# Kernel tuning notes

Measured on AMD Instinct MI355X. Metric: run time of the kernel, lower is better.

The kernel has to match this reference:

```python
import jax, jax.numpy as jnp
import numpy as np
from jax import lax

NUM_CLASSES = 91
C_FEAT = 2048
HF = WF = 16          # backbone feature map size (512px image / stride 32)
STRIDE = 32           # anchor stride, as in source generate_base_anchors
N_ANCHOR_TYPES = 9
NMS_THR = 0.5
K_ROIS = 100          # fixed proposal count after NMS (padded, jit-safe)
SPATIAL_SCALE = 1.0 / 16.0
POOL = 7
SR = 2                # sampling ratio (source uses adaptive -1; fixed here)


def conv2d(x, w, b, pad):
    y = lax.conv_general_dilated(x, w, (1, 1), pad,
                                 dimension_numbers=('NCHW', 'OIHW', 'NCHW'))
    return y + b[None, :, None, None]


def setup_inputs():
    key = jax.random.key(0)
    ks = jax.random.split(key, 16)
    f32 = jnp.float32
    def w(k, shape, s=0.01):
        return jax.random.normal(k, shape, f32) * s
    z = lambda n: jnp.zeros((n,), f32)
    D = C_FEAT * POOL * POOL  # 100352
    return dict(
        x=jax.random.normal(ks[0], (1, C_FEAT, HF, WF), f32),
        rpn_w=w(ks[1], (512, C_FEAT, 3, 3)), rpn_b=z(512),
        cls_w=w(ks[2], (18, 512, 1, 1)), cls_b=z(18),
        bbox_w=w(ks[3], (36, 512, 1, 1)), bbox_b=z(36),
        fc1c_w=w(ks[4], (D, 4096)), fc1c_b=z(4096),
        fc2c_w=w(ks[5], (4096, NUM_CLASSES)), fc2c_b=z(NUM_CLASSES),
        fc1b_w=w(ks[6], (D, 4096)), fc1b_b=z(4096),
        fc2b_w=w(ks[7], (4096, 4)), fc2b_b=z(4),
        m1_w=w(ks[8], (256, C_FEAT, 3, 3)), m1_b=z(256),
        mt_w=w(ks[9], (256, 256, 2, 2)), mt_b=z(256),  # ConvT weight [C_in,C_out,kh,kw]
        m2_w=w(ks[10], (1, 256, 1, 1)), m2_b=z(1),
    )


def _anchors(hf, wf):
    scales = jnp.array([8.0, 16.0, 32.0])
    ratios = jnp.array([0.5, 1.0, 2.0])
    ws = (scales[:, None] * jnp.sqrt(ratios)[None, :]).reshape(-1)  # scale-major, 9
    hs = (scales[:, None] / jnp.sqrt(ratios)[None, :]).reshape(-1)
    base = jnp.stack([-ws / 2, -hs / 2, ws / 2, hs / 2], axis=1)    # [9,4]
    sy, sx = jnp.meshgrid(jnp.arange(hf) * STRIDE, jnp.arange(wf) * STRIDE, indexing='ij')
    shifts = jnp.stack([sx, sy, sx, sy], -1).reshape(-1, 4).astype(jnp.float32)  # [HW,4]
    return (base[:, None, :] + shifts[None, :, :]).reshape(-1, 4)   # [9*HW,4] anchor-type major


def _decode(a, d):
    wa = a[:, 2] - a[:, 0]
    ha = a[:, 3] - a[:, 1]
    cx = a[:, 0] + 0.5 * wa
    cy = a[:, 1] + 0.5 * ha
    px = cx + d[:, 0] * wa
    py = cy + d[:, 1] * ha
    pw = jnp.exp(d[:, 2]) * wa
    ph = jnp.exp(d[:, 3]) * ha
    return jnp.stack([px - 0.5 * pw, py - 0.5 * ph, px + 0.5 * pw, py + 0.5 * ph], 1)


def _nms_topk(boxes, scores, thr, k):
    n = boxes.shape[0]
    order = jnp.argsort(-scores)
    b = boxes[order]
    s = scores[order]
    area = (b[:, 2] - b[:, 0]) * (b[:, 3] - b[:, 1])
    xx1 = jnp.maximum(b[:, None, 0], b[None, :, 0])
    yy1 = jnp.maximum(b[:, None, 1], b[None, :, 1])
    xx2 = jnp.minimum(b[:, None, 2], b[None, :, 2])
    yy2 = jnp.minimum(b[:, None, 3], b[None, :, 3])
    inter = jnp.clip(xx2 - xx1, 0) * jnp.clip(yy2 - yy1, 0)
    iou = inter / (area[:, None] + area[None, :] - inter + 1e-9)
    j = jnp.arange(n)
    def body(i, keep):
        sup = keep[i] & (iou[i] > thr) & (j > i)
        return keep & ~sup
    keep = lax.fori_loop(0, n, body, jnp.ones((n,), bool))
    masked = jnp.where(keep, s, -jnp.inf)
    vals, pos = lax.top_k(masked, k)
    valid = jnp.isfinite(vals)
    fb = jnp.where(valid[:, None], b[pos], 0.0)
    fs = jnp.where(valid, vals, 0.0)
    return fb, fs


def _roi_align(feat, boxes):
    # feat: [C,H,W]; boxes: [K,4] in image coords
    C, H, W = feat.shape
    r = boxes * SPATIAL_SCALE
    S = POOL * SR  # 14 sample points per side
    t = (jnp.arange(S, dtype=feat.dtype) + 0.5) / S
    gx = jnp.clip(r[:, 0:1] + t[None, :] * (r[:, 2:3] - r[:, 0:1]), 0.0, W - 1.0)
    gy = jnp.clip(r[:, 1:2] + t[None, :] * (r[:, 3:4] - r[:, 1:2]), 0.0, H - 1.0)
    x0 = jnp.floor(gx); y0 = jnp.floor(gy)
    lx = gx - x0; ly = gy - y0
    x0i = x0.astype(jnp.int32); y0i = y0.astype(jnp.int32)
    x1i = jnp.minimum(x0i + 1, W - 1); y1i = jnp.minimum(y0i + 1, H - 1)
    flat = feat.reshape(C, H * W)
    def g(yi, xi):  # yi:[K,S] row coords, xi:[K,S] col coords -> [C,K,S,S]
        idx = yi[:, :, None] * W + xi[:, None, :]
        return flat[:, idx]
    lyb = ly[:, :, None]; lxb = lx[:, None, :]
    v = ((1 - lyb) * (1 - lxb) * g(y0i, x0i)
         + (1 - lyb) * lxb * g(y0i, x1i)
         + lyb * (1 - lxb) * g(y1i, x0i)
         + lyb * lxb * g(y1i, x1i))  # [C,K,S,S]
    v = v.reshape(C, -1, POOL, SR, POOL, SR).mean(axis=(3, 5))
    return v.transpose(1, 0, 2, 3)  # [K,C,7,7]


def reference(x, rpn_w, rpn_b, cls_w, cls_b, bbox_w, bbox_b,
              fc1c_w, fc1c_b, fc2c_w, fc2c_b,
              fc1b_w, fc1b_b, fc2b_w, fc2b_b,
              m1_w, m1_b, mt_w, mt_b, m2_w, m2_b):
    p1 = [(1, 1), (1, 1)]; p0 = [(0, 0), (0, 0)]
    f = jax.nn.relu(conv2d(x, rpn_w, rpn_b, p1))      # [1,512,H,W]
    obj = conv2d(f, cls_w, cls_b, p0)                 # [1,18,H,W]
    deltas = conv2d(f, bbox_w, bbox_b, p0)            # [1,36,H,W]
    hf, wf = f.shape[2], f.shape[3]
    hw = hf * wf
    # softmax over the 2 objectness classes (view(B,2,-1) layout)
    scores = jax.nn.softmax(obj.reshape(2, N_ANCHOR_TYPES, hw), axis=0)[1].reshape(-1)
    d = deltas.reshape(N_ANCHOR_TYPES, 4, hw).transpose(0, 2, 1).reshape(-1, 4)
    anchors = _anchors(hf, wf)
    boxes = _decode(anchors, d)
    fb, fs = _nms_topk(boxes, scores, NMS_THR, K_ROIS)
    rois = _roi_align(x[0], fb)                       # [K,2048,7,7]
    flat = rois.reshape(K_ROIS, -1)
    cls_out = jax.nn.relu(flat @ fc1c_w + fc1c_b) @ fc2c_w + fc2c_b
    box_out = jax.nn.relu(flat @ fc1b_w + fc1b_b) @ fc2b_w + fc2b_b
    m = jax.nn.relu(conv2d(rois, m1_w, m1_b, p1))     # [K,256,7,7]
    # ConvTranspose2d(k=2,s=2): non-overlapping, each pixel expands to a 2x2 block
    up = jnp.einsum('nchw,coij->nohiwj', m, mt_w).reshape(K_ROIS, 256, 2 * POOL, 2 * POOL)
    m = jax.nn.relu(up + mt_b[None, :, None, None])
    masks = conv2d(m, m2_w, m2_b, p0)                 # [K,1,14,14]
    return cls_out, box_out, masks
```

## Files before the change

### kernel.cpp

```cpp
#include <hip/hip_runtime.h>

#define DEVFN __device__ __forceinline__

typedef unsigned short ushort_t;
typedef unsigned int uint32;
typedef __attribute__((ext_vector_type(8))) short bf16x8;
typedef __attribute__((ext_vector_type(4))) float f32x4;

typedef __attribute__((address_space(3))) unsigned int lds_uint;
typedef const __attribute__((address_space(1))) unsigned int glob_uint;

DEVFN ushort_t f2bf(float x) {
    uint32 b = __float_as_uint(x);
    uint32 r = (b + 0x7FFFu + ((b >> 16) & 1u)) >> 16;
    return (ushort_t)r;
}
DEVFN float bf2f(ushort_t u) { return __uint_as_float(((uint32)u) << 16); }

union BWU { uint32 u[4]; bf16x8 v8; };

__global__ __launch_bounds__(256) void k_pre(const float* __restrict__ x,
                                             const float* __restrict__ rpn_w,
                                             float* __restrict__ fpart,
                                             const float* __restrict__ m1_w,
                                             const float* __restrict__ mt_w,
                                             ushort_t* __restrict__ wAf,
                                             ushort_t* __restrict__ wA2f,
                                             float* __restrict__ xt) {
    const int bid = blockIdx.x, tid = threadIdx.x;
    if (bid < 1024) {
        __shared__ float xs[8][18][18];
        const int coP = bid & 127, ks = bid >> 7;
        const int ty = tid >> 4, tx = tid & 15;
        const int co0 = coP * 4;
        for (int i = tid; i < 8 * 18 * 18; i += 256) ((float*)xs)[i] = 0.f;
        float acc[4] = {0.f, 0.f, 0.f, 0.f};
        for (int ch = 0; ch < 32; ++ch) {
            const int cib = ks * 256 + ch * 8;
            __syncthreads();
#pragma unroll
            for (int cc = 0; cc < 8; ++cc) xs[cc][ty + 1][tx + 1] = x[(size_t)(cib + cc) * 256 + tid];
            __syncthreads();
#pragma unroll
            for (int cc = 0; cc < 8; ++cc) {
                const int ci = cib + cc;
                float v[9];
#pragma unroll
                for (int t = 0; t < 9; ++t) v[t] = xs[cc][ty + t / 3][tx + t % 3];
                const float* wb = rpn_w + ((size_t)co0 * 2048 + ci) * 9;
#pragma unroll
                for (int o = 0; o < 4; ++o) {
                    const float* w = wb + (size_t)o * 2048 * 9;
#pragma unroll
                    for (int t = 0; t < 9; ++t) acc[o] = fmaf(v[t], w[t], acc[o]);
                }
            }
        }
#pragma unroll
        for (int o = 0; o < 4; ++o) fpart[((size_t)ks * 512 + co0 + o) * 256 + tid] = acc[o];
        return;
    }
    const int pb = bid - 1024;
    if (pb < 256) {
        const int p = pb * 4 + (tid >> 6);
        const int lane = tid & 63, l15 = lane & 15, lg = lane >> 4;
        const int cot = p >> 6, cis = p & 63;
        const int co = cot * 16 + l15, k0 = cis * 32 + lg * 8;
        const float* src = m1_w + ((size_t)co * 2048 + k0) * 9;
        float v[72];
#pragma unroll
        for (int i = 0; i < 72; ++i) v[i] = src[i];
#pragma unroll
        for (int tap = 0; tap < 9; ++tap) {
            ushort_t* dst = wAf + ((size_t)((tap * 16 + cot) * 64 + cis) * 512) + lane * 8;
            ushort_t t8[8];
#pragma unroll
            for (int j = 0; j < 8; ++j) t8[j] = f2bf(v[j * 9 + tap]);
            uint4 u;
            u.x = (uint32)t8[0] | ((uint32)t8[1] << 16);
            u.y = (uint32)t8[2] | ((uint32)t8[3] << 16);
            u.z = (uint32)t8[4] | ((uint32)t8[5] << 16);
            u.w = (uint32)t8[6] | ((uint32)t8[7] << 16);
            *(uint4*)dst = u;
        }
    } else if (pb < 1280) {
        int idx = (pb - 256) * 256 + tid;
        int j = idx & 7, lane = (idx >> 3) & 63, cis = (idx >> 9) & 7, cot = idx >> 12;
        int row = cot * 16 + (lane & 15);
        int c = cis * 32 + (lane >> 4) * 8 + j;
        int o = row >> 2, ij = row & 3;
        wA2f[idx] = f2bf(mt_w[((size_t)c * 256 + o) * 4 + ij]);
    } else {
        int pos = pb - 1280;
        for (int i = 0; i < 8; ++i) {
            int c = tid + i * 256;
            xt[(size_t)pos * 2048 + c] = x[(size_t)c * 256 + pos];
        }
    }
}

__global__ void k_rpn_reduce(const float* __restrict__ fpart, const float* __restrict__ rpn_b,
                             float* __restrict__ f) {
    const int i = blockIdx.x * 256 + threadIdx.x;
    float s = 0.f;
#pragma unroll
    for (int p = 0; p < 8; ++p) s += fpart[(size_t)p * 131072 + i];
    f[i] = fmaxf(s + rpn_b[i >> 8], 0.f);
}

__global__ void k_head(const float* __restrict__ f, const float* __restrict__ cls_w,
                       const float* __restrict__ cls_b, const float* __restrict__ bbox_w,
                       const float* __restrict__ bbox_b, float* __restrict__ scores,
                       float* __restrict__ boxes) {
    const int a = blockIdx.x, pos = threadIdx.x;
    float o0 = 0, o1 = 0, d0 = 0, d1 = 0, d2 = 0, d3 = 0;
    const float* c0 = cls_w + (size_t)a * 512;
    const float* c1 = cls_w + (size_t)(9 + a) * 512;
    const float* b0p = bbox_w + (size_t)(4 * a) * 512;
    const float* b1p = b0p + 512;
    const float* b2p = b0p + 1024;
    const float* b3p = b0p + 1536;
    for (int ci = 0; ci < 512; ci += 8) {
        float fv[8];
#pragma unroll
        for (int j = 0; j < 8; ++j) fv[j] = f[(size_t)(ci + j) * 256 + pos];
#pragma unroll
        for (int j = 0; j < 8; ++j) {
            o0 = fmaf(c0[ci + j], fv[j], o0);
            o1 = fmaf(c1[ci + j], fv[j], o1);
            d0 = fmaf(b0p[ci + j], fv[j], d0);
            d1 = fmaf(b1p[ci + j], fv[j], d1);
            d2 = fmaf(b2p[ci + j], fv[j], d2);
            d3 = fmaf(b3p[ci + j], fv[j], d3);
        }
    }
    o0 += cls_b[a]; o1 += cls_b[9 + a];
    d0 += bbox_b[4 * a + 0]; d1 += bbox_b[4 * a + 1];
    d2 += bbox_b[4 * a + 2]; d3 += bbox_b[4 * a + 3];
    float mx = fmaxf(o0, o1);
    float e0 = expf(o0 - mx), e1 = expf(o1 - mx);
    float sc = e1 / (e0 + e1);
    int si = a / 3, ri = a % 3;
    float scale = (si == 0) ? 8.f : ((si == 1) ? 16.f : 32.f);
    float ratio = (ri == 0) ? 0.5f : ((ri == 1) ? 1.f : 2.f);
    float sq = sqrtf(ratio);
    float hw2 = (scale * sq) * 0.5f;
    float hh2 = (scale / sq) * 0.5f;
    int py = pos >> 4, px = pos & 15;
    float sx = (float)(px * 32), sy = (float)(py * 32);
    float a0 = sx - hw2, a1 = sy - hh2, a2 = sx + hw2, a3 = sy + hh2;
    float wa = a2 - a0, ha = a3 - a1;
    float cx = a0 + 0.5f * wa, cy = a1 + 0.5f * ha;
    float pxc = cx + d0 * wa, pyc = cy + d1 * ha;
    float pw = expf(d2) * wa, ph = expf(d3) * ha;
    int idx = a * 256 + pos;
    scores[idx] = sc;
    boxes[idx * 4 + 0] = pxc - 0.5f * pw;
    boxes[idx * 4 + 1] = pyc - 0.5f * ph;
    boxes[idx * 4 + 2] = pxc + 0.5f * pw;
    boxes[idx * 4 + 3] = pyc + 0.5f * ph;
}

__global__ void k_sort(const float* __restrict__ scores, const float* __restrict__ boxes,
                       float* __restrict__ ssort, float* __restrict__ bsort) {
    const int i = blockIdx.x * 256 + threadIdx.x;
    const float si = scores[i];
    int rank = 0;
    for (int j = 0; j < 2304; ++j) {
        float sj = scores[j];
        rank += (sj > si) || (sj == si && j < i);
    }
    ssort[rank] = si;
    float4 bb = *(const float4*)(boxes + (size_t)i * 4);
    *(float4*)(bsort + (size_t)rank * 4) = bb;
}

__global__ void k_adj(const float* __restrict__ bsort, unsigned long long* __restrict__ adj) {
    const int i = blockIdx.x, lane = threadIdx.x;
    const float4 bi = *(const float4*)(bsort + (size_t)i * 4);
    const float ai = (bi.z - bi.x) * (bi.w - bi.y);
    for (int w = 0; w < 36; ++w) {
        int j = w * 64 + lane;
        bool sup = false;
        if (j < 2304 && j > i) {
            float4 bj = *(const float4*)(bsort + (size_t)j * 4);
            float aj = (bj.z - bj.x) * (bj.w - bj.y);
            float xx1 = fmaxf(bi.x, bj.x), yy1 = fmaxf(bi.y, bj.y);
            float xx2 = fminf(bi.z, bj.z), yy2 = fminf(bi.w, bj.w);
            float inter = fmaxf(xx2 - xx1, 0.f) * fmaxf(yy2 - yy1, 0.f);
            float iou = inter / (ai + aj - inter + 1e-9f);
            sup = iou > 0.5f;
        }
        unsigned long long m = __ballot(sup);
        if (lane == 0) adj[(size_t)i * 36 + w] = m;
    }
}

__global__ void k_nms(const unsigned long long* __restrict__ adj, const float* __restrict__ bsort,
                      float* __restrict__ fb) {
    const int lane = threadIdx.x;
    unsigned long long r = (lane < 36) ? 0ULL : ~0ULL;
    int cnt = 0;
    for (int it = 0; it < 128; ++it) {
        unsigned long long inv = ~r;
        int local = inv ? (__ffsll((unsigned long long)inv) - 1) : 64;
        int cand = (local < 64) ? lane * 64 + local : (1 << 30);
#pragma unroll
        for (int d = 32; d; d >>= 1) cand = min(cand, __shfl_xor(cand, d));
        if (cand >= 2304) break;
        if (lane == 0) *(float4*)(fb + (size_t)cnt * 4) = *(const float4*)(bsort + (size_t)cand * 4);
        ++cnt;
        if (cnt == 100) break;
        unsigned long long a = (lane < 36) ? adj[(size_t)cand * 36 + lane] : 0ULL;
        r |= a;
        if (lane == (cand >> 6)) r |= 1ULL << (cand & 63);
    }
    for (int s2 = lane; s2 < 100; s2 += 64)
        if (s2 >= cnt) {
            float4 z = {0.f, 0.f, 0.f, 0.f};
            *(float4*)(fb + (size_t)s2 * 4) = z;
        }
}

__global__ __launch_bounds__(256) void k_roi(const float* __restrict__ xt,
                                             const float* __restrict__ fb,
                                             ushort_t* __restrict__ flatA,
                                             ushort_t* __restrict__ flatT) {
    __shared__ int sxi0[14], sxi1[14], syi0[14], syi1[14];
    __shared__ float slx[14], sly[14];
    const int cg = blockIdx.x, n = blockIdx.y, tid = threadIdx.x;
    const float r0 = fb[n * 4 + 0] * 0.0625f, r1 = fb[n * 4 + 1] * 0.0625f;
    const float r2 = fb[n * 4 + 2] * 0.0625f, r3 = fb[n * 4 + 3] * 0.0625f;
    if (tid < 14) {
        float tt = ((float)tid + 0.5f) * (1.0f / 14.0f);
        float gx = r0 + tt * (r2 - r0);
        gx = fminf(fmaxf(gx, 0.f), 15.f);
        float x0f = floorf(gx);
        int x0 = (int)x0f;
        sxi0[tid] = x0; sxi1[tid] = min(x0 + 1, 15); slx[tid] = gx - x0f;
        float gy = r1 + tt * (r3 - r1);
        gy = fminf(fmaxf(gy, 0.f), 15.f);
        float y0f = floorf(gy);
        int y0 = (int)y0f;
        syi0[tid] = y0; syi1[tid] = min(y0 + 1, 15); sly[tid] = gy - y0f;
    }
    __syncthreads();
    const int c = cg * 256 + tid;
    for (int py = 0; py < 7; ++py) {
        for (int px = 0; px < 7; ++px) {
            float accv = 0.f;
#pragma unroll
            for (int a2 = 0; a2 < 2; ++a2) {
                int sy = py * 2 + a2;
                int y0 = syi0[sy], y1 = syi1[sy];
                float ly = sly[sy];
#pragma unroll
                for (int b2 = 0; b2 < 2; ++b2) {
                    int sx = px * 2 + b2;
                    int x0 = sxi0[sx], x1 = sxi1[sx];
                    float lx = slx[sx];
                    float v00 = xt[(size_t)(y0 * 16 + x0) * 2048 + c];
                    float v01 = xt[(size_t)(y0 * 16 + x1) * 2048 + c];
                    float v10 = xt[(size_t)(y1 * 16 + x0) * 2048 + c];
                    float v11 = xt[(size_t)(y1 * 16 + x1) * 2048 + c];
                    accv += (1.f - ly) * (1.f - lx) * v00 + (1.f - ly) * lx * v01 +
                            ly * (1.f - lx) * v10 + ly * lx * v11;
                }
            }
            ushort_t bv = f2bf(accv * 0.25f);
            int pos = py * 7 + px;
            flatT[((size_t)n * 49 + pos) * 2048 + c] = bv;
            int k = c * 49 + pos;
            flatA[((size_t)(k >> 5) * 112 + n) * 32 + (k & 31)] = bv;
        }
    }
}

__global__ __launch_bounds__(256) void k_big(const ushort_t* __restrict__ flatA,
                                             const ushort_t* __restrict__ flatT,
                                             const float* __restrict__ Wc,
                                             const float* __restrict__ Wb,
                                             float* __restrict__ part,
                                             const ushort_t* __restrict__ wAf,
                                             const float* __restrict__ m1_b,
                                             ushort_t* __restrict__ m1outT) {
    __shared__ float wlds[2][32][128];
    const int bid = blockIdx.x, tid = threadIdx.x;
    const int wave = tid >> 6, lane = tid & 63, l15 = lane & 15, lg = lane >> 4;
    const f32x4 zz = {0.f, 0.f, 0.f, 0.f};
    if (bid < 77) {
        const int nb = bid;
        int nn[4], ppy[4], ppx[4], colv[4];
#pragma unroll
        for (int nt = 0; nt < 4; ++nt) {
            int col = nb * 64 + nt * 16 + l15;
            colv[nt] = col;
            int n = col / 49;
            int pos = col - n * 49;
            nn[nt] = n;
            ppy[nt] = pos / 7;
            ppx[nt] = pos - (pos / 7) * 7;
        }
        f32x4 acc[4][4];
#pragma unroll
        for (int a = 0; a < 4; ++a)
#pragma unroll
            for (int b = 0; b < 4; ++b) acc[a][b] = zz;
        bf16x8 zfrag;
#pragma unroll
        for (int j = 0; j < 8; ++j) zfrag[j] = 0;
        for (int tap = 0; tap < 9; ++tap) {
            const int ty = tap / 3 - 1, tx = tap % 3 - 1;
            int val[4];
            size_t bofs[4];
#pragma unroll
            for (int nt = 0; nt < 4; ++nt) {
                int iy = ppy[nt] + ty, ix = ppx[nt] + tx;
                val[nt] = (iy >= 0 && iy < 7 && ix >= 0 && ix < 7);
                bofs[nt] = ((size_t)nn[nt] * 49 + iy * 7 + ix) * 2048;
            }
            for (int cis = 0; cis < 64; ++cis) {
                const int kq = cis * 32 + lg * 8;
                bf16x8 a[4];
#pragma unroll
                for (int mt = 0; mt < 4; ++mt)
                    a[mt] = *(const bf16x8*)(wAf +
                            ((size_t)((tap * 16 + wave * 4 + mt) * 64 + cis) * 64 + lane) * 8);
                bf16x8 b[4];
#pragma unroll
                for (int nt = 0; nt < 4; ++nt)
                    b[nt] = val[nt] ? *(const bf16x8*)(flatT + bofs[nt] + kq) : zfrag;
#pragma unroll
                for (int nt = 0; nt < 4; ++nt)
#pragma unroll
                    for (int mt = 0; mt < 4; ++mt)
                        acc[mt][nt] = __builtin_amdgcn_mfma_f32_16x16x32_bf16(a[mt], b[nt], acc[mt][nt], 0, 0, 0);
            }
        }
#pragma unroll
        for (int mt = 0; mt < 4; ++mt)
#pragma unroll
            for (int nt = 0; nt < 4; ++nt) {
                int co0 = wave * 64 + mt * 16 + lg * 4;
                ushort_t v[4];
#pragma unroll
                for (int r = 0; r < 4; ++r)
                    v[r] = f2bf(fmaxf(acc[mt][nt][r] + m1_b[co0 + r], 0.f));
                uint2 u;
                u.x = (uint32)v[0] | ((uint32)v[1] << 16);
                u.y = (uint32)v[2] | ((uint32)v[3] << 16);
                *(uint2*)(m1outT + (size_t)colv[nt] * 256 + co0) = u;
            }
        return;
    }
    const int h = bid - 77;
    const int x = h & 7, t = h >> 3;
    const int colTile = t >> 2, rem = t & 3;
    const int kc = x * 2 + (rem & 1), br = rem >> 1;
    const float* W = br ? Wb : Wc;
    const int ncol0 = colTile * 128 + wave * 32;
    const float* wbase = W + (size_t)(kc * 6272) * 4096 + colTile * 128;
    const int srow = lane >> 5, scol = (lane & 31) * 4;

    auto stage = [&](int buf, int s) {
        const float* g0 = wbase + ((size_t)(s * 32 + wave * 8 + srow)) * 4096 + scol;
#pragma unroll
        for (int q = 0; q < 4; ++q) {
            const float* g = g0 + (size_t)(q * 2) * 4096;
            float* l = &wlds[buf][wave * 8 + q * 2][0];
            __builtin_amdgcn_global_load_lds((glob_uint*)g, (lds_uint*)l, 16, 0, 0);
        }
    };

    f32x4 acc0[7], acc1[7];
#pragma unroll
    for (int tt = 0; tt < 7; ++tt) { acc0[tt] = zz; acc1[tt] = zz; }

    const ushort_t* ap = flatA + ((size_t)(kc * 196) * 112 + l15) * 32 + lg * 8;
    stage(0, 0);
    bf16x8 afc[7];
#pragma unroll
    for (int tt = 0; tt < 7; ++tt) afc[tt] = *(const bf16x8*)(ap + (size_t)tt * 512);
    asm volatile("s_waitcnt vmcnt(0)" ::: "memory");
    __builtin_amdgcn_sched_barrier(0);
    __builtin_amdgcn_s_barrier();
    __builtin_amdgcn_sched_barrier(0);

    for (int s = 0; s < 196; ++s) {
        const int b = s & 1;
        bf16x8 afn[7];
        if (s + 1 < 196) {
            const ushort_t* apn = ap + 3584;
#pragma unroll
            for (int tt = 0; tt < 7; ++tt) afn[tt] = *(const bf16x8*)(apn + (size_t)tt * 512);
            stage(b ^ 1, s + 1);
            asm volatile("s_waitcnt vmcnt(11)" ::: "memory");
        } else {
#pragma unroll
            for (int tt = 0; tt < 7; ++tt) afn[tt] = afc[tt];
            asm volatile("s_waitcnt vmcnt(0)" ::: "memory");
        }
        __builtin_amdgcn_sched_barrier(0);
        __builtin_amdgcn_s_barrier();
        __builtin_amdgcn_sched_barrier(0);
        const float* wrow = &wlds[b][lg * 8][wave * 32 + l15];
        BWU b0u, b1u;
#pragma unroll
        for (int i = 0; i < 4; ++i) {
            float w0a = wrow[(2 * i) * 128], w0b = wrow[(2 * i + 1) * 128];
            float w1a = wrow[(2 * i) * 128 + 16], w1b = wrow[(2 * i + 1) * 128 + 16];
            asm("v_cvt_pk_bf16_f32 %0, %1, %2" : "=v"(b0u.u[i]) : "v"(w0a), "v"(w0b));
            asm("v_cvt_pk_bf16_f32 %0, %1, %2" : "=v"(b1u.u[i]) : "v"(w1a), "v"(w1b));
        }
#pragma unroll
        for (int tt = 0; tt < 7; ++tt) {
            acc0[tt] = __builtin_amdgcn_mfma_f32_16x16x32_bf16(afc[tt], b0u.v8, acc0[tt], 0, 0, 0);
            acc1[tt] = __builtin_amdgcn_mfma_f32_16x16x32_bf16(afc[tt], b1u.v8, acc1[tt], 0, 0, 0);
        }
        __builtin_amdgcn_sched_barrier(0);
        __builtin_amdgcn_s_barrier();
        __builtin_amdgcn_sched_barrier(0);
#pragma unroll
        for (int tt = 0; tt < 7; ++tt) afc[tt] = afn[tt];
        ap += 3584;
    }
    float* pb = part + (size_t)(br * 16 + kc) * 112 * 4096;
#pragma unroll
    for (int tt = 0; tt < 7; ++tt)
#pragma unroll
        for (int r = 0; r < 4; ++r) {
            int m = tt * 16 + lg * 4 + r;
            pb[(size_t)m * 4096 + ncol0 + l15] = acc0[tt][r];
            pb[(size_t)m * 4096 + ncol0 + 16 + l15] = acc1[tt][r];
        }
}

__global__ __launch_bounds__(256) void k_fc2(const float* __restrict__ part,
                                             const float* __restrict__ fc1c_b,
                                             const float* __restrict__ fc1b_b,
                                             const float* __restrict__ Wc,
                                             const float* __restrict__ bc,
                                             const float* __restrict__ Wb,
                                             const float* __restrict__ bb,
                                             float* __restrict__ out) {
    __shared__ float h_s[2][4096];
    __shared__ float ph[2][91];
    __shared__ float pbx[2][4];
    const int m = blockIdx.x, tid = threadIdx.x;
    for (int i = tid; i < 8192; i += 256) {
        int br = i >> 12, col = i & 4095;
        float s = br ? fc1b_b[col] : fc1c_b[col];
#pragma unroll
        for (int p = 0; p < 16; ++p) s += part[((size_t)(br * 16 + p) * 112 + m) * 4096 + col];
        h_s[br][col] = fmaxf(s, 0.f);
    }
    __syncthreads();
    const int half = tid >> 7, col = tid & 127;
    if (col < 91) {
        const float* hrow = &h_s[0][half * 2048];
        const float* wp = Wc + (size_t)half * 2048 * 91 + col;
        float a0 = 0, a1 = 0, a2 = 0, a3 = 0, a4 = 0, a5 = 0, a6 = 0, a7 = 0;
        for (int k = 0; k < 2048; k += 8) {
            a0 = fmaf(hrow[k],     wp[(size_t)k * 91], a0);
            a1 = fmaf(hrow[k + 1], wp[(size_t)(k + 1) * 91], a1);
            a2 = fmaf(hrow[k + 2], wp[(size_t)(k + 2) * 91], a2);
            a3 = fmaf(hrow[k + 3], wp[(size_t)(k + 3) * 91], a3);
            a4 = fmaf(hrow[k + 4], wp[(size_t)(k + 4) * 91], a4);
            a5 = fmaf(hrow[k + 5], wp[(size_t)(k + 5) * 91], a5);
            a6 = fmaf(hrow[k + 6], wp[(size_t)(k + 6) * 91], a6);
            a7 = fmaf(hrow[k + 7], wp[(size_t)(k + 7) * 91], a7);
        }
        ph[half][col] = ((a0 + a1) + (a2 + a3)) + ((a4 + a5) + (a6 + a7));
    } else if (col >= 96 && col < 100) {
        int bcol = col - 96;
        const float* hrow = &h_s[1][half * 2048];
        const float* wp = Wb + (size_t)half * 2048 * 4 + bcol;
        float a0 = 0, a1 = 0, a2 = 0, a3 = 0, a4 = 0, a5 = 0, a6 = 0, a7 = 0;
        for (int k = 0; k < 2048; k += 8) {
            a0 = fmaf(hrow[k],     wp[(size_t)k * 4], a0);
            a1 = fmaf(hrow[k + 1], wp[(size_t)(k + 1) * 4], a1);
            a2 = fmaf(hrow[k + 2], wp[(size_t)(k + 2) * 4], a2);
            a3 = fmaf(hrow[k + 3], wp[(size_t)(k + 3) * 4], a3);
            a4 = fmaf(hrow[k + 4], wp[(size_t)(k + 4) * 4], a4);
            a5 = fmaf(hrow[k + 5], wp[(size_t)(k + 5) * 4], a5);
            a6 = fmaf(hrow[k + 6], wp[(size_t)(k + 6) * 4], a6);
            a7 = fmaf(hrow[k + 7], wp[(size_t)(k + 7) * 4], a7);
        }
        pbx[half][bcol] = ((a0 + a1) + (a2 + a3)) + ((a4 + a5) + (a6 + a7));
    }
    __syncthreads();
    if (tid < 91) out[m * 91 + tid] = bc[tid] + ph[0][tid] + ph[1][tid];
    else if (tid >= 96 && tid < 100) {
        int bcol = tid - 96;
        out[9100 + m * 4 + bcol] = bb[bcol] + pbx[0][bcol] + pbx[1][bcol];
    }
}

__global__ __launch_bounds__(256) void k_up(const ushort_t* __restrict__ m1outT,
                                            const ushort_t* __restrict__ wA2f,
                                            ushort_t* __restrict__ upT) {
    const int nb = blockIdx.x, cq = blockIdx.y, tid = threadIdx.x;
    const int wave = tid >> 6, lane = tid & 63, l15 = lane & 15, lg = lane >> 4;
    int colv[4];
#pragma unroll
    for (int nt = 0; nt < 4; ++nt) colv[nt] = nb * 64 + nt * 16 + l15;
    f32x4 acc[4][4];
    const f32x4 zz = {0.f, 0.f, 0.f, 0.f};
#pragma unroll
    for (int a = 0; a < 4; ++a)
#pragma unroll
        for (int b = 0; b < 4; ++b) acc[a][b] = zz;
    for (int cis = 0; cis < 8; ++cis) {
        const int kq = cis * 32 + lg * 8;
        bf16x8 a[4];
#pragma unroll
        for (int mt = 0; mt < 4; ++mt)
            a[mt] = *(const bf16x8*)(wA2f +
                    ((size_t)((cq * 16 + wave * 4 + mt) * 8 + cis) * 64 + lane) * 8);
        bf16x8 b[4];
#pragma unroll
        for (int nt = 0; nt < 4; ++nt)
            b[nt] = *(const bf16x8*)(m1outT + (size_t)colv[nt] * 256 + kq);
#pragma unroll
        for (int nt = 0; nt < 4; ++nt)
#pragma unroll
            for (int mt = 0; mt < 4; ++mt)
                acc[mt][nt] = __builtin_amdgcn_mfma_f32_16x16x32_bf16(a[mt], b[nt], acc[mt][nt], 0, 0, 0);
    }
#pragma unroll
    for (int mt = 0; mt < 4; ++mt)
#pragma unroll
        for (int nt = 0; nt < 4; ++nt) {
            int rb = (cq * 16 + wave * 4 + mt) * 16 + lg * 4;
            ushort_t v[4];
#pragma unroll
            for (int r = 0; r < 4; ++r) v[r] = f2bf(acc[mt][nt][r]);
            uint2 u;
            u.x = (uint32)v[0] | ((uint32)v[1] << 16);
            u.y = (uint32)v[2] | ((uint32)v[3] << 16);
            *(uint2*)(upT + (size_t)colv[nt] * 1024 + rb) = u;
        }
}

__global__ void k_mask(const ushort_t* __restrict__ upT, const float* __restrict__ mt_b,
                       const float* __restrict__ m2_w, const float* __restrict__ m2_b,
                       float* __restrict__ out) {
    const int n = blockIdx.x, t = threadIdx.x;
    if (t >= 196) return;
    const int ys = t / 14, xs = t % 14;
    const int ro = (ys & 1) * 2 + (xs & 1);
    const int col = n * 49 + (ys >> 1) * 7 + (xs >> 1);
    const ushort_t* up0 = upT + (size_t)col * 1024 + ro;
    float a0 = m2_b[0], a1 = 0.f, a2 = 0.f, a3 = 0.f;
#pragma unroll 4
    for (int o = 0; o < 256; o += 4) {
        a0 = fmaf(m2_w[o],     fmaxf(bf2f(up0[(o) * 4]) + mt_b[o], 0.f), a0);
        a1 = fmaf(m2_w[o + 1], fmaxf(bf2f(up0[(o + 1) * 4]) + mt_b[o + 1], 0.f), a1);
        a2 = fmaf(m2_w[o + 2], fmaxf(bf2f(up0[(o + 2) * 4]) + mt_b[o + 2], 0.f), a2);
        a3 = fmaf(m2_w[o + 3], fmaxf(bf2f(up0[(o + 3) * 4]) + mt_b[o + 3], 0.f), a3);
    }
    out[9500 + n * 196 + t] = (a0 + a1) + (a2 + a3);
}

extern "C" void kernel_launch(void* const* d_in, const int* in_sizes, int n_in,
                              void* d_out, int out_size, void* d_ws, size_t ws_size,
                              hipStream_t stream) {
    const float* x      = (const float*)d_in[0];
    const float* rpn_w  = (const float*)d_in[1];
    const float* rpn_b  = (const float*)d_in[2];
    const float* cls_w  = (const float*)d_in[3];
    const float* cls_b  = (const float*)d_in[4];
    const float* bbox_w = (const float*)d_in[5];
    const float* bbox_b = (const float*)d_in[6];
    const float* fc1c_w = (const float*)d_in[7];
    const float* fc1c_b = (const float*)d_in[8];
    const float* fc2c_w = (const float*)d_in[9];
    const float* fc2c_b = (const float*)d_in[10];
    const float* fc1b_w = (const float*)d_in[11];
    const float* fc1b_b = (const float*)d_in[12];
    const float* fc2b_w = (const float*)d_in[13];
    const float* fc2b_b = (const float*)d_in[14];
    const float* m1_w   = (const float*)d_in[15];
    const float* m1_b   = (const float*)d_in[16];
    const float* mt_w   = (const float*)d_in[17];
    const float* mt_b   = (const float*)d_in[18];
    const float* m2_w   = (const float*)d_in[19];
    const float* m2_b   = (const float*)d_in[20];
    float* out = (float*)d_out;

    char* ws = (char*)d_ws;
    size_t off = 0;
    auto take = [&](size_t nbytes) -> char* {
        char* p = ws + off;
        off += (nbytes + 255) & ~(size_t)255;
        return p;
    };
    float* xt      = (float*)take(2097152);
    float* fpart   = (float*)take(4194304);
    float* f       = (float*)take(524288);
    float* scores  = (float*)take(9216);
    float* boxes   = (float*)take(36864);
    float* ssort   = (float*)take(9216);
    float* bsort   = (float*)take(36864);
    unsigned long long* adj = (unsigned long long*)take(663552);
    float* fb      = (float*)take(1600);
    ushort_t* flatA = (ushort_t*)take(22478848);
    ushort_t* flatT = (ushort_t*)take(20471808);
    float* part1   = (float*)take(58720256);
    ushort_t* wAf  = (ushort_t*)take(9437184);
    ushort_t* m1outT = (ushort_t*)take(2523136);
    ushort_t* wA2f = (ushort_t*)take(524288);
    ushort_t* upT  = (ushort_t*)part1;

    k_pre<<<2560, 256, 0, stream>>>(x, rpn_w, fpart, m1_w, mt_w, wAf, wA2f, xt);
    k_rpn_reduce<<<512, 256, 0, stream>>>(fpart, rpn_b, f);
    k_head<<<9, 256, 0, stream>>>(f, cls_w, cls_b, bbox_w, bbox_b, scores, boxes);
    k_sort<<<9, 256, 0, stream>>>(scores, boxes, ssort, bsort);
    k_adj<<<2304, 64, 0, stream>>>(bsort, adj);
    k_nms<<<1, 64, 0, stream>>>(adj, bsort, fb);
    k_roi<<<dim3(8, 100), 256, 0, stream>>>(xt, fb, flatA, flatT);
    k_big<<<1101, 256, 0, stream>>>(flatA, flatT, fc1c_w, fc1b_w, part1, wAf, m1_b, m1outT);
    k_fc2<<<100, 256, 0, stream>>>(part1, fc1c_b, fc1b_b, fc2c_w, fc2c_b, fc2b_w, fc2b_b, out);
    k_up<<<dim3(77, 4), 256, 0, stream>>>(m1outT, wA2f, upT);
    k_mask<<<100, 256, 0, stream>>>(upT, mt_b, m2_w, m2_b, out);
}
```

Baseline: 1.487 ms.

## Triple-buffer fc1 weight staging, reorder K to position-major, cache NMS adjacency in LDS

The fc1 GEMM now uses a three-deep LDS ring with two stages of weight loads in flight, and unrolls the loop by two to alternate A-register buffers. The reduction order over K changes to position-major: flatA is written with a (pos, channel-group) index and weight rows are gathered with stride 49. Each weight stage therefore reads rows 49 apart instead of contiguous rows, which may hurt DRAM locality. NMS also copies the first 224 rows of the adjacency matrix into LDS, so the serial suppression loop avoids global latency for top-ranked candidates.

```diff
diff --git a/kernel.cpp b/kernel.cpp
--- a/kernel.cpp
+++ b/kernel.cpp
@@ -198,7 +198,10 @@
 
 __global__ void k_nms(const unsigned long long* __restrict__ adj, const float* __restrict__ bsort,
                       float* __restrict__ fb) {
+    __shared__ unsigned long long adjL[224 * 36];
     const int lane = threadIdx.x;
+    for (int i = lane; i < 224 * 36; i += 64) adjL[i] = adj[i];
+    __syncthreads();
     unsigned long long r = (lane < 36) ? 0ULL : ~0ULL;
     int cnt = 0;
     for (int it = 0; it < 128; ++it) {
@@ -211,7 +214,8 @@
         if (lane == 0) *(float4*)(fb + (size_t)cnt * 4) = *(const float4*)(bsort + (size_t)cand * 4);
         ++cnt;
         if (cnt == 100) break;
-        unsigned long long a = (lane < 36) ? adj[(size_t)cand * 36 + lane] : 0ULL;
+        unsigned long long a = 0ULL;
+        if (lane < 36) a = (cand < 224) ? adjL[cand * 36 + lane] : adj[(size_t)cand * 36 + lane];
         r |= a;
         if (lane == (cand >> 6)) r |= 1ULL << (cand & 63);
     }
@@ -270,8 +274,8 @@
             ushort_t bv = f2bf(accv * 0.25f);
             int pos = py * 7 + px;
             flatT[((size_t)n * 49 + pos) * 2048 + c] = bv;
-            int k = c * 49 + pos;
-            flatA[((size_t)(k >> 5) * 112 + n) * 32 + (k & 31)] = bv;
+            int sg = pos * 64 + (c >> 5);
+            flatA[((size_t)sg * 112 + n) * 32 + (c & 31)] = bv;
         }
     }
 }
@@ -284,7 +288,7 @@
                                              const ushort_t* __restrict__ wAf,
                                              const float* __restrict__ m1_b,
                                              ushort_t* __restrict__ m1outT) {
-    __shared__ float wlds[2][32][128];
+    __shared__ float wlds[3][32][128];
     const int bid = blockIdx.x, tid = threadIdx.x;
     const int wave = tid >> 6, lane = tid & 63, l15 = lane & 15, lg = lane >> 4;
     const f32x4 zz = {0.f, 0.f, 0.f, 0.f};
@@ -359,51 +363,22 @@
     const int kc = x * 2 + (rem & 1), br = rem >> 1;
     const float* W = br ? Wb : Wc;
     const int ncol0 = colTile * 128 + wave * 32;
-    const float* wbase = W + (size_t)(kc * 6272) * 4096 + colTile * 128;
+    const int colOff = colTile * 128;
     const int srow = lane >> 5, scol = (lane & 31) * 4;
 
-    auto stage = [&](int buf, int s) {
-        const float* g0 = wbase + ((size_t)(s * 32 + wave * 8 + srow)) * 4096 + scol;
+    auto stage = [&](int buf, int S) {
+        const int pos = S >> 6;
+        const int c0 = (S & 63) * 32;
+        const int rbase = c0 + wave * 8 + srow;
 #pragma unroll
         for (int q = 0; q < 4; ++q) {
-            const float* g = g0 + (size_t)(q * 2) * 4096;
+            const float* g = W + (size_t)((rbase + q * 2) * 49 + pos) * 4096 + colOff + scol;
             float* l = &wlds[buf][wave * 8 + q * 2][0];
             __builtin_amdgcn_global_load_lds((glob_uint*)g, (lds_uint*)l, 16, 0, 0);
         }
     };
-
-    f32x4 acc0[7], acc1[7];
-#pragma unroll
-    for (int tt = 0; tt < 7; ++tt) { acc0[tt] = zz; acc1[tt] = zz; }
-
-    const ushort_t* ap = flatA + ((size_t)(kc * 196) * 112 + l15) * 32 + lg * 8;
-    stage(0, 0);
-    bf16x8 afc[7];
-#pragma unroll
-    for (int tt = 0; tt < 7; ++tt) afc[tt] = *(const bf16x8*)(ap + (size_t)tt * 512);
-    asm volatile("s_waitcnt vmcnt(0)" ::: "memory");
-    __builtin_amdgcn_sched_barrier(0);
-    __builtin_amdgcn_s_barrier();
-    __builtin_amdgcn_sched_barrier(0);
-
-    for (int s = 0; s < 196; ++s) {
-        const int b = s & 1;
-        bf16x8 afn[7];
-        if (s + 1 < 196) {
-            const ushort_t* apn = ap + 3584;
-#pragma unroll
-            for (int tt = 0; tt < 7; ++tt) afn[tt] = *(const bf16x8*)(apn + (size_t)tt * 512);
-            stage(b ^ 1, s + 1);
-            asm volatile("s_waitcnt vmcnt(11)" ::: "memory");
-        } else {
-#pragma unroll
-            for (int tt = 0; tt < 7; ++tt) afn[tt] = afc[tt];
-            asm volatile("s_waitcnt vmcnt(0)" ::: "memory");
-        }
-        __builtin_amdgcn_sched_barrier(0);
-        __builtin_amdgcn_s_barrier();
-        __builtin_amdgcn_sched_barrier(0);
-        const float* wrow = &wlds[b][lg * 8][wave * 32 + l15];
+    auto compute = [&](int buf, const bf16x8* af, f32x4* a0p, f32x4* a1p) {
+        const float* wrow = &wlds[buf][lg * 8][wave * 32 + l15];
         BWU b0u, b1u;
 #pragma unroll
         for (int i = 0; i < 4; ++i) {
@@ -414,15 +389,71 @@
         }
 #pragma unroll
         for (int tt = 0; tt < 7; ++tt) {
-            acc0[tt] = __builtin_amdgcn_mfma_f32_16x16x32_bf16(afc[tt], b0u.v8, acc0[tt], 0, 0, 0);
-            acc1[tt] = __builtin_amdgcn_mfma_f32_16x16x32_bf16(afc[tt], b1u.v8, acc1[tt], 0, 0, 0);
-        }
-        __builtin_amdgcn_sched_barrier(0);
-        __builtin_amdgcn_s_barrier();
-        __builtin_amdgcn_sched_barrier(0);
-#pragma unroll
-        for (int tt = 0; tt < 7; ++tt) afc[tt] = afn[tt];
-        ap += 3584;
+            a0p[tt] = __builtin_amdgcn_mfma_f32_16x16x32_bf16(af[tt], b0u.v8, a0p[tt], 0, 0, 0);
+            a1p[tt] = __builtin_amdgcn_mfma_f32_16x16x32_bf16(af[tt], b1u.v8, a1p[tt], 0, 0, 0);
+        }
+    };
+
+    f32x4 acc0[7], acc1[7];
+#pragma unroll
+    for (int tt = 0; tt < 7; ++tt) { acc0[tt] = zz; acc1[tt] = zz; }
+
+    const int Sbase = kc * 196;
+    const ushort_t* ap = flatA + ((size_t)Sbase * 112 + l15) * 32 + lg * 8;
+    stage(0, Sbase);
+    stage(1, Sbase + 1);
+    bf16x8 afA[7], afB[7];
+#pragma unroll
+    for (int tt = 0; tt < 7; ++tt) afA[tt] = *(const bf16x8*)(ap + (size_t)tt * 512);
+    asm volatile("s_waitcnt vmcnt(4)" ::: "memory");
+    __builtin_amdgcn_sched_barrier(0);
+    __builtin_amdgcn_s_barrier();
+    __builtin_amdgcn_sched_barrier(0);
+
+    for (int su = 0; su < 98; ++su) {
+        const int s0 = 2 * su, s1 = 2 * su + 1;
+        {
+            const ushort_t* apn = ap + 3584;
+#pragma unroll
+            for (int tt = 0; tt < 7; ++tt) afB[tt] = *(const bf16x8*)(apn + (size_t)tt * 512);
+            if (s0 + 2 < 196) {
+                stage((s0 + 2) % 3, Sbase + s0 + 2);
+                asm volatile("s_waitcnt vmcnt(15)" ::: "memory");
+            } else {
+                asm volatile("s_waitcnt vmcnt(11)" ::: "memory");
+            }
+            __builtin_amdgcn_sched_barrier(0);
+            __builtin_amdgcn_s_barrier();
+            __builtin_amdgcn_sched_barrier(0);
+            compute(s0 % 3, afA, acc0, acc1);
+            __builtin_amdgcn_sched_barrier(0);
+            __builtin_amdgcn_s_barrier();
+            __builtin_amdgcn_sched_barrier(0);
+            ap += 3584;
+        }
+        {
+            if (s1 + 1 < 196) {
+                const ushort_t* apn = ap + 3584;
+#pragma unroll
+                for (int tt = 0; tt < 7; ++tt) afA[tt] = *(const bf16x8*)(apn + (size_t)tt * 512);
+            }
+            if (s1 + 2 < 196) {
+                stage((s1 + 2) % 3, Sbase + s1 + 2);
+                asm volatile("s_waitcnt vmcnt(15)" ::: "memory");
+            } else if (s1 + 1 < 196) {
+                asm volatile("s_waitcnt vmcnt(11)" ::: "memory");
+            } else {
+                asm volatile("s_waitcnt vmcnt(0)" ::: "memory");
+            }
+            __builtin_amdgcn_sched_barrier(0);
+            __builtin_amdgcn_s_barrier();
+            __builtin_amdgcn_sched_barrier(0);
+            compute(s1 % 3, afB, acc0, acc1);
+            __builtin_amdgcn_sched_barrier(0);
+            __builtin_amdgcn_s_barrier();
+            __builtin_amdgcn_sched_barrier(0);
+            ap += 3584;
+        }
     }
     float* pb = part + (size_t)(br * 16 + kc) * 112 * 4096;
 #pragma unroll
```

Result: no change. 1.497 ms (+0.7%).
